# Optimization experiments

Hardware: AMD Instinct MI355X
Metric: run time of the kernel (lower is better)

Reference implementation:

```python
import jax, jax.numpy as jnp
import numpy as np

B, T, C, K = 16, 4096, 64, 1024  # K = codebook rows including pad row 0


def setup_inputs() -> dict:
    key = jax.random.key(0)
    k1, k2, k3 = jax.random.split(key, 3)
    z = jax.random.normal(k1, (B, T, C), dtype=jnp.float32)
    codebook_weight = jax.random.normal(k2, (K, C), dtype=jnp.float32)
    # contiguous valid prefixes of random length (torch loop breaks at first 0)
    lengths = jax.random.randint(k3, (B,), T // 2, T + 1)
    mask = (jnp.arange(T)[None, :] < lengths[:, None]).astype(jnp.float32)[:, :, None]
    return {"z": z, "codebook_weight": codebook_weight, "mask": mask}


def _forward(z, codebook_weight, mask):
    # F.normalize(z, p=2, dim=-1) with eps clamp
    z = z / jnp.clip(jnp.linalg.norm(z, axis=-1, keepdims=True), 1e-12)
    e = jax.lax.stop_gradient(codebook_weight)[1:]  # (K-1, C), detached like torch
    zf = z.reshape(-1, C)                            # (B*T, C)
    # squared euclidean distances: ||z||^2 + ||e||^2 - 2 z e^T
    d = (zf * zf).sum(1, keepdims=True) + (e * e).sum(1)[None, :] - 2.0 * (zf @ e.T)
    idx = jnp.argmin(d, axis=1).reshape(B, T)        # (B, T) codes in [0, K-2]
    # scatter(one-hot) @ e  ==  gather rows of e
    z_q = e[idx] * mask                              # (B, T, C)

    valid_count = mask.sum()
    commitment_loss = (jnp.square(z - jax.lax.stop_gradient(z_q)) * mask).sum() / valid_count

    # straight-through estimator
    z_q = z + z_q - jax.lax.stop_gradient(z)

    m1 = mask[:, 1:, :]
    smoothness_loss = (jnp.square(z_q[:, :-1, :] - z_q[:, 1:, :]) * m1).sum() / m1.sum()

    # --- parallel RLE (replaces the host-side python loop) ---
    # torch loop breaks at first mask==0 -> only contiguous valid prefix matters
    mvalid = jnp.cumprod(mask[..., 0], axis=1) > 0   # (B, T) bool
    change = idx[:, 1:] != idx[:, :-1]
    # position 0 always starts a segment; new segment where code changes inside valid prefix
    is_start = jnp.concatenate(
        [jnp.ones((B, 1), dtype=bool), change & mvalid[:, 1:]], axis=1)  # (B, T)
    # stable argsort puts start positions first, in increasing time order
    order = jnp.argsort(jnp.where(is_start, 0, 1), axis=1)               # (B, T)
    n = is_start.sum(axis=1)                                             # segments per batch
    sel_mask = jnp.arange(T)[None, :] < n[:, None]                        # (B, T)
    sel_pos = jnp.where(sel_mask, order, 0)                               # padded to T
    n_mask = sel_mask.astype(jnp.float32)[..., None]                      # (B, T, 1)
    n_z_q = jnp.take_along_axis(z_q, sel_pos[:, :, None], axis=1) * n_mask
    selected_encodings = jnp.where(
        sel_mask, jnp.take_along_axis(idx, sel_pos, axis=1) + 1, 0)       # (B, T) int
    return smoothness_loss, commitment_loss, z_q, n_z_q, n_mask, selected_encodings


def reference(z, codebook_weight, mask):
    return _forward(z, codebook_weight, mask)
```

## Files before the change

kernel.cpp:

```cpp
#include <hip/hip_runtime.h>
#include <math.h>

typedef __attribute__((ext_vector_type(8))) short short8;
typedef __attribute__((ext_vector_type(4))) float f32x4;

#define B_  16
#define T_  4096
#define C_  64
#define KE_ 1023
#define BT_ (B_ * T_)
#define WINHALF 5e-4f


__device__ __forceinline__ unsigned short f2bf(float x) {
    unsigned int u = __float_as_uint(x);
    unsigned int r = (u + 0x7FFFu + ((u >> 16) & 1u)) >> 16;
    return (unsigned short)r;
}
__device__ __forceinline__ float bf2f(unsigned short h) {
    return __uint_as_float(((unsigned int)h) << 16);
}

typedef __attribute__((address_space(1))) const unsigned int g_u32;
typedef __attribute__((address_space(3))) unsigned int l_u32;
__device__ __forceinline__ void gload16(const void* g, void* l) {
    __builtin_amdgcn_global_load_lds((g_u32*)g, (l_u32*)l, 16, 0, 0);
}

__global__ __launch_bounds__(256) void k_prep(const float* __restrict__ cb,
                                              float* __restrict__ ee,
                                              float* __restrict__ ee2,
                                              unsigned short* __restrict__ Eh,
                                              unsigned short* __restrict__ El,
                                              int* __restrict__ flagcnt) {
    const int gid = blockIdx.x * 256 + threadIdx.x;
    const int k = gid >> 5;
    const int c = gid & 31;
    if (gid == 0) *flagcnt = 0;
    unsigned int* EhU = (unsigned int*)Eh;
    unsigned int* ElU = (unsigned int*)El;
    if (k < KE_) {
        const float x0 = cb[(size_t)(k + 1) * C_ + 2 * c];
        const float x1 = cb[(size_t)(k + 1) * C_ + 2 * c + 1];
        const float n0 = -x0, n1 = -x1;
        const unsigned short h0 = f2bf(n0), h1 = f2bf(n1);
        const unsigned short l0 = f2bf(n0 - bf2f(h0));
        const unsigned short l1 = f2bf(n1 - bf2f(h1));
        EhU[k * 32 + c] = (unsigned int)h0 | ((unsigned int)h1 << 16);
        ElU[k * 32 + c] = (unsigned int)l0 | ((unsigned int)l1 << 16);
        if (c == 0) {
            const float* r = cb + (size_t)(k + 1) * C_;
            float s = 0.f;
            #pragma unroll
            for (int cc = 0; cc < C_; cc += 2) {
                const float y0 = r[cc], y1 = r[cc + 1];
                s = fmaf(y0, y0, s);
                s = fmaf(y1, y1, s);
            }
            ee[k]  = s;
            ee2[k] = 0.5f + 0.5f * s;
        }
    } else {
        EhU[k * 32 + c] = 0u;
        ElU[k * 32 + c] = 0u;
        if (c == 0) { ee[k] = INFINITY; ee2[k] = INFINITY; }
    }
}

__global__ __launch_bounds__(256, 2) void k_assign(
    const float* __restrict__ z, const unsigned short* __restrict__ Eh,
    const unsigned short* __restrict__ El, const float* __restrict__ ee2,
    int* __restrict__ kbest, int* __restrict__ flaglist,
    int* __restrict__ flagcnt) {

    __shared__ __align__(16) unsigned short s_eh[2][128 * 64];
    __shared__ __align__(16) unsigned short s_el[2][128 * 64];
    __shared__ float s_ee[2][128];

    const int tid  = threadIdx.x;
    const int wave = tid >> 6;
    const int lane = tid & 63;
    const int col  = lane & 15;
    const int quad = lane >> 4;
    const int Q0   = blockIdx.x * 128 + wave * 32;

    short8 ah[2][2], al[2][2];
    #pragma unroll
    for (int g = 0; g < 2; ++g) {
        const float4* zp = (const float4*)(z + (size_t)(Q0 + g * 16 + col) * C_);
        const float4 f0 = zp[quad * 2];
        const float4 f1 = zp[quad * 2 + 1];
        const float4 f2 = zp[8 + quad * 2];
        const float4 f3 = zp[8 + quad * 2 + 1];
        float xs[16] = {f0.x, f0.y, f0.z, f0.w, f1.x, f1.y, f1.z, f1.w,
                        f2.x, f2.y, f2.z, f2.w, f3.x, f3.y, f3.z, f3.w};
        float ss = 0.f;
        #pragma unroll
        for (int i = 0; i < 16; ++i) ss = fmaf(xs[i], xs[i], ss);
        ss += __shfl_xor(ss, 16);
        ss += __shfl_xor(ss, 32);
        const float inv = 1.f / fmaxf(sqrtf(ss), 1e-12f);
        short8 h0, h1, l0, l1;
        #pragma unroll
        for (int i = 0; i < 8; ++i) {
            const float x = xs[i] * inv;
            const unsigned short hx = f2bf(x);
            h0[i] = (short)hx;
            l0[i] = (short)f2bf(x - bf2f(hx));
            const float y = xs[8 + i] * inv;
            const unsigned short hy = f2bf(y);
            h1[i] = (short)hy;
            l1[i] = (short)f2bf(y - bf2f(hy));
        }
        ah[g][0] = h0; ah[g][1] = h1;
        al[g][0] = l0; al[g][1] = l1;
    }

    float bestv[2][4], secv[2][4];
    int   bkk[2][4];
    #pragma unroll
    for (int g = 0; g < 2; ++g)
        #pragma unroll
        for (int r = 0; r < 4; ++r) {
            bestv[g][r] = INFINITY; secv[g][r] = INFINITY; bkk[g][r] = 0;
        }

    const int srow = tid >> 3;
    const int schk = (tid & 7) ^ (srow & 7);
    const int ldsb = (wave * 8) * 64;

#define STAGE_J(tt, bb, j) do {                                                \
        const size_t go = (size_t)((tt) * 128 + (j) * 32 + srow) * 64          \
                          + (size_t)schk * 8;                                  \
        gload16(Eh + go, (void*)&s_eh[bb][ldsb + (j) * 2048]);                 \
        gload16(El + go, (void*)&s_el[bb][ldsb + (j) * 2048]);                 \
    } while (0)

    int cur = 0;
    #pragma unroll
    for (int j = 0; j < 4; ++j) STAGE_J(0, 0, j);
    if (tid < 128) s_ee[0][tid] = ee2[tid];
    __syncthreads();

    const int coff = (quad ^ (col & 7)) * 8;

    for (int t = 0; t < 8; ++t) {
        if (t < 7) { STAGE_J(t + 1, cur ^ 1, 0); STAGE_J(t + 1, cur ^ 1, 1); }

        float ev[8];
        #pragma unroll
        for (int s = 0; s < 8; ++s) ev[s] = s_ee[cur][s * 16 + col];

        short8 fh0 = *(const short8*)&s_eh[cur][col * 64 + coff];
        short8 fh1 = *(const short8*)&s_eh[cur][col * 64 + (coff ^ 32)];
        short8 fl0 = *(const short8*)&s_el[cur][col * 64 + coff];
        short8 fl1 = *(const short8*)&s_el[cur][col * 64 + (coff ^ 32)];

        if (t < 7) {
            STAGE_J(t + 1, cur ^ 1, 2); STAGE_J(t + 1, cur ^ 1, 3);
            if (tid < 128) s_ee[cur ^ 1][tid] = ee2[(t + 1) * 128 + tid];
        }

        const int kb = t * 128 + col;

        #pragma unroll
        for (int s = 0; s < 8; ++s) {
            const int sn = (s < 7) ? (s + 1) : 7;
            const int rb = (sn * 16 + col) * 64;
            short8 nh0 = *(const short8*)&s_eh[cur][rb + coff];
            short8 nh1 = *(const short8*)&s_eh[cur][rb + (coff ^ 32)];
            short8 nl0 = *(const short8*)&s_el[cur][rb + coff];
            short8 nl1 = *(const short8*)&s_el[cur][rb + (coff ^ 32)];

            const float e2 = ev[s];
            f32x4 p0a = {e2, e2, e2, e2}, p0b = {0.f, 0.f, 0.f, 0.f};
            f32x4 p1a = {e2, e2, e2, e2}, p1b = {0.f, 0.f, 0.f, 0.f};
            __builtin_amdgcn_s_setprio(1);
            p0a = __builtin_amdgcn_mfma_f32_16x16x32_bf16(ah[0][0], fh0, p0a, 0, 0, 0);
            p1a = __builtin_amdgcn_mfma_f32_16x16x32_bf16(ah[1][0], fh0, p1a, 0, 0, 0);
            p0b = __builtin_amdgcn_mfma_f32_16x16x32_bf16(ah[0][1], fl1, p0b, 0, 0, 0);
            p1b = __builtin_amdgcn_mfma_f32_16x16x32_bf16(ah[1][1], fl1, p1b, 0, 0, 0);
            p0a = __builtin_amdgcn_mfma_f32_16x16x32_bf16(ah[0][1], fh1, p0a, 0, 0, 0);
            p1a = __builtin_amdgcn_mfma_f32_16x16x32_bf16(ah[1][1], fh1, p1a, 0, 0, 0);
            p0b = __builtin_amdgcn_mfma_f32_16x16x32_bf16(al[0][0], fh0, p0b, 0, 0, 0);
            p1b = __builtin_amdgcn_mfma_f32_16x16x32_bf16(al[1][0], fh0, p1b, 0, 0, 0);
            p0a = __builtin_amdgcn_mfma_f32_16x16x32_bf16(ah[0][0], fl0, p0a, 0, 0, 0);
            p1a = __builtin_amdgcn_mfma_f32_16x16x32_bf16(ah[1][0], fl0, p1a, 0, 0, 0);
            p0b = __builtin_amdgcn_mfma_f32_16x16x32_bf16(al[0][1], fh1, p0b, 0, 0, 0);
            p1b = __builtin_amdgcn_mfma_f32_16x16x32_bf16(al[1][1], fh1, p1b, 0, 0, 0);
            __builtin_amdgcn_s_setprio(0);

            const int kc = kb + s * 16;
            #pragma unroll
            for (int r = 0; r < 4; ++r) {
                {
                    const float v  = p0a[r] + p0b[r];
                    const float bo = bestv[0][r];
                    bkk[0][r]   = (v < bo) ? kc : bkk[0][r];
                    secv[0][r]  = fminf(secv[0][r], fmaxf(bo, v));
                    bestv[0][r] = fminf(bo, v);
                }
                {
                    const float v  = p1a[r] + p1b[r];
                    const float bo = bestv[1][r];
                    bkk[1][r]   = (v < bo) ? kc : bkk[1][r];
                    secv[1][r]  = fminf(secv[1][r], fmaxf(bo, v));
                    bestv[1][r] = fminf(bo, v);
                }
            }
            fh0 = nh0; fh1 = nh1; fl0 = nl0; fl1 = nl1;
        }
        __syncthreads();
        cur ^= 1;
    }
#undef STAGE_J

    #pragma unroll
    for (int g = 0; g < 2; ++g) {
        #pragma unroll
        for (int r = 0; r < 4; ++r) {
            float b  = bestv[g][r], sc = secv[g][r];
            int   k  = bkk[g][r];
            #pragma unroll
            for (int off = 1; off < 16; off <<= 1) {
                const float ob = __shfl_xor(b, off);
                const int   ok = __shfl_xor(k, off);
                const float os = __shfl_xor(sc, off);
                const bool take = (ob < b) || (ob == b && ok < k);
                const float lose = take ? b : ob;
                sc = fminf(fminf(sc, os), lose);
                b  = take ? ob : b;
                k  = take ? ok : k;
            }
            if (col == 0) {
                const int q = Q0 + g * 16 + quad * 4 + r;
                kbest[q] = k;
                if (!(sc - b > WINHALF)) {
                    const int pos = atomicAdd(flagcnt, 1);
                    flaglist[pos] = q;
                }
            }
        }
    }
}

__global__ __launch_bounds__(256) void k_fix(const float* __restrict__ z,
                                             const float* __restrict__ cb,
                                             const float* __restrict__ ee,
                                             const int* __restrict__ flagcnt,
                                             const int* __restrict__ flaglist,
                                             int* __restrict__ kbest) {
    __shared__ float s_z[64];
    __shared__ float s_bv[4];
    __shared__ int   s_bk[4];
    const int tid  = threadIdx.x;
    const int lane = tid & 63;
    const int wave = tid >> 6;
    const int n = *flagcnt;

    for (int i = blockIdx.x; i < n; i += 1024) {
        const int q = flaglist[i];
        __syncthreads();
        if (tid < 16) ((float4*)s_z)[tid] = ((const float4*)(z + (size_t)q * C_))[tid];
        __syncthreads();

        float4 zn[16];
        float ss = 0.f;
        #pragma unroll
        for (int c4 = 0; c4 < 16; ++c4) {
            const float4 v = ((const float4*)s_z)[c4];
            zn[c4] = v;
            ss = fmaf(v.x, v.x, ss); ss = fmaf(v.y, v.y, ss);
            ss = fmaf(v.z, v.z, ss); ss = fmaf(v.w, v.w, ss);
        }
        const float nrm = fmaxf(sqrtf(ss), 1e-12f);
        #pragma unroll
        for (int c4 = 0; c4 < 16; ++c4) {
            zn[c4].x /= nrm; zn[c4].y /= nrm; zn[c4].z /= nrm; zn[c4].w /= nrm;
        }

        const int k0 = tid * 4;
        const float4* e0 = (const float4*)(cb + (size_t)(k0 + 1) * C_);
        const float4* e1 = (const float4*)(cb + (size_t)(k0 + 2) * C_);
        const float4* e2 = (const float4*)(cb + (size_t)(k0 + 3) * C_);
        const float4* e3 = (const float4*)(cb + (size_t)((k0 + 4 <= KE_) ? (k0 + 4) : KE_) * C_);
        float d0 = 0.f, d1 = 0.f, d2 = 0.f, d3 = 0.f;
        #pragma unroll
        for (int c4 = 0; c4 < 16; ++c4) {
            const float4 x = zn[c4];
            const float4 a = e0[c4], b = e1[c4], c = e2[c4], d = e3[c4];
            d0 = fmaf(x.x, a.x, d0); d0 = fmaf(x.y, a.y, d0);
            d0 = fmaf(x.z, a.z, d0); d0 = fmaf(x.w, a.w, d0);
            d1 = fmaf(x.x, b.x, d1); d1 = fmaf(x.y, b.y, d1);
            d1 = fmaf(x.z, b.z, d1); d1 = fmaf(x.w, b.w, d1);
            d2 = fmaf(x.x, c.x, d2); d2 = fmaf(x.y, c.y, d2);
            d2 = fmaf(x.z, c.z, d2); d2 = fmaf(x.w, c.w, d2);
            d3 = fmaf(x.x, d.x, d3); d3 = fmaf(x.y, d.y, d3);
            d3 = fmaf(x.z, d.z, d3); d3 = fmaf(x.w, d.w, d3);
        }
        float bv = INFINITY;
        int   bk = 0;
        float v;
        v = fmaf(-2.f, d0, ee[k0 + 0]); if (v < bv) { bv = v; bk = k0 + 0; }
        v = fmaf(-2.f, d1, ee[k0 + 1]); if (v < bv) { bv = v; bk = k0 + 1; }
        v = fmaf(-2.f, d2, ee[k0 + 2]); if (v < bv) { bv = v; bk = k0 + 2; }
        v = fmaf(-2.f, d3, ee[k0 + 3]); if (v < bv) { bv = v; bk = k0 + 3; }

        #pragma unroll
        for (int off = 32; off > 0; off >>= 1) {
            const float ov = __shfl_down(bv, off);
            const int   ok = __shfl_down(bk, off);
            if (ov < bv || (ov == bv && ok < bk)) { bv = ov; bk = ok; }
        }
        if (lane == 0) { s_bv[wave] = bv; s_bk[wave] = bk; }
        __syncthreads();
        if (tid == 0) {
            float fb = s_bv[0]; int fk = s_bk[0];
            #pragma unroll
            for (int w = 1; w < 4; ++w) {
                if (s_bv[w] < fb || (s_bv[w] == fb && s_bk[w] < fk)) {
                    fb = s_bv[w]; fk = s_bk[w];
                }
            }
            kbest[q] = fk;
        }
    }
}

__global__ __launch_bounds__(256) void k_episcan(
    const float* __restrict__ z, const float* __restrict__ cb,
    const float* __restrict__ mask, const int* __restrict__ kbest,
    float* __restrict__ zqo,
    float* __restrict__ commit_part, float* __restrict__ valid_part,
    float* __restrict__ smooth_part,
    int* __restrict__ selpos, int* __restrict__ nst) {

    const int tid = threadIdx.x;

    if (blockIdx.x < 16) {
        __shared__ int cnt[256];
        const int b = blockIdx.x;
        const int base = b * T_;
        const int t0 = tid * 16;

        int flags = 0, c = 0;
        int prev = (tid == 0) ? -1 : kbest[base + t0 - 1];
        #pragma unroll
        for (int i = 0; i < 16; ++i) {
            const int t = t0 + i;
            const int cur = kbest[base + t];
            const int is = (t == 0) ? 1
                         : ((cur != prev && mask[base + t] > 0.f) ? 1 : 0);
            flags |= is << i;
            c += is;
            prev = cur;
        }
        cnt[tid] = c;
        __syncthreads();
        for (int off = 1; off < 256; off <<= 1) {
            int add = (tid >= off) ? cnt[tid - off] : 0;
            __syncthreads();
            cnt[tid] += add;
            __syncthreads();
        }
        int pos = cnt[tid] - c;
        #pragma unroll
        for (int i = 0; i < 16; ++i) {
            if ((flags >> i) & 1) selpos[base + pos++] = t0 + i;
        }
        if (tid == 255) nst[b] = cnt[255];
        return;
    }

    __shared__ float s_red[12];
    const int bid  = blockIdx.x - 16;
    const int lane = tid & 63;
    const int wave = tid >> 6;
    const int gt   = bid * 256 + tid;
    const int q    = gt >> 2;
    const int p    = gt & 3;
    const int grp  = lane >> 2;

    const int bi = kbest[q];
    const float m = mask[q];

    const float4* zp = (const float4*)(z + (size_t)q * C_ + p * 16);
    const float4* er = (const float4*)(cb + (size_t)(bi + 1) * C_ + p * 16);
    float4* zo = (float4*)(zqo + (size_t)q * C_ + p * 16);

    float4 zr[4];
    float ss = 0.f;
    #pragma unroll
    for (int i = 0; i < 4; ++i) {
        float4 v = zp[i];
        zr[i] = v;
        ss = fmaf(v.x, v.x, ss); ss = fmaf(v.y, v.y, ss);
        ss = fmaf(v.z, v.z, ss); ss = fmaf(v.w, v.w, ss);
    }
    ss += __shfl_xor(ss, 1);
    ss += __shfl_xor(ss, 2);
    const float nrm = fmaxf(sqrtf(ss), 1e-12f);

    float commit = 0.f, sm = 0.f;
    float4 ov[4];
    #pragma unroll
    for (int c4 = 0; c4 < 4; ++c4) {
        const float z0 = zr[c4].x / nrm, z1 = zr[c4].y / nrm;
        const float z2 = zr[c4].z / nrm, z3 = zr[c4].w / nrm;
        const float4 e4 = er[c4];
        const float q0 = e4.x * m, q1 = e4.y * m, q2 = e4.z * m, q3 = e4.w * m;
        float4 o;
        o.x = (z0 + q0) - z0;
        o.y = (z1 + q1) - z1;
        o.z = (z2 + q2) - z2;
        o.w = (z3 + q3) - z3;
        zo[c4] = o;
        ov[c4] = o;
        const float d0 = z0 - q0, d1 = z1 - q1, d2 = z2 - q2, d3 = z3 - q3;
        commit = fmaf(d0, d0, commit); commit = fmaf(d1, d1, commit);
        commit = fmaf(d2, d2, commit); commit = fmaf(d3, d3, commit);
    }
    commit *= m;

    float mnext = 0.f;
    if (grp != 15) mnext = mask[q + 1];
    #pragma unroll
    for (int c4 = 0; c4 < 4; ++c4) {
        const float n0 = __shfl_down(ov[c4].x, 4);
        const float n1 = __shfl_down(ov[c4].y, 4);
        const float n2 = __shfl_down(ov[c4].z, 4);
        const float n3 = __shfl_down(ov[c4].w, 4);
        const float x0 = ov[c4].x - n0, x1 = ov[c4].y - n1;
        const float x2 = ov[c4].z - n2, x3 = ov[c4].w - n3;
        sm = fmaf(x0, x0, sm); sm = fmaf(x1, x1, sm);
        sm = fmaf(x2, x2, sm); sm = fmaf(x3, x3, sm);
    }
    sm *= mnext;

    if (grp == 15) {
        float mn = 0.f;
        if ((q & (T_ - 1)) != T_ - 1) mn = mask[q + 1];
        if (mn > 0.f) {
            const int bi2 = kbest[q + 1];
            const float4* zp2 = (const float4*)(z + (size_t)(q + 1) * C_ + p * 16);
            const float4* er2 = (const float4*)(cb + (size_t)(bi2 + 1) * C_ + p * 16);
            float4 zr2[4];
            float s2 = 0.f;
            #pragma unroll
            for (int i = 0; i < 4; ++i) {
                float4 v = zp2[i];
                zr2[i] = v;
                s2 = fmaf(v.x, v.x, s2); s2 = fmaf(v.y, v.y, s2);
                s2 = fmaf(v.z, v.z, s2); s2 = fmaf(v.w, v.w, s2);
            }
            s2 += __shfl_xor(s2, 1);
            s2 += __shfl_xor(s2, 2);
            const float nrm2 = fmaxf(sqrtf(s2), 1e-12f);
            float smb = 0.f;
            #pragma unroll
            for (int c4 = 0; c4 < 4; ++c4) {
                const float w0 = zr2[c4].x / nrm2, w1 = zr2[c4].y / nrm2;
                const float w2 = zr2[c4].z / nrm2, w3 = zr2[c4].w / nrm2;
                const float4 e4 = er2[c4];
                const float a0 = e4.x * mn, a1 = e4.y * mn;
                const float a2 = e4.z * mn, a3 = e4.w * mn;
                const float o0 = (w0 + a0) - w0;
                const float o1 = (w1 + a1) - w1;
                const float o2 = (w2 + a2) - w2;
                const float o3 = (w3 + a3) - w3;
                const float x0 = ov[c4].x - o0, x1 = ov[c4].y - o1;
                const float x2 = ov[c4].z - o2, x3 = ov[c4].w - o3;
                smb = fmaf(x0, x0, smb); smb = fmaf(x1, x1, smb);
                smb = fmaf(x2, x2, smb); smb = fmaf(x3, x3, smb);
            }
            sm = smb * mn;
        }
    }

    float vc = (p == 0) ? m : 0.f;
    #pragma unroll
    for (int off = 32; off > 0; off >>= 1) {
        commit += __shfl_down(commit, off);
        vc     += __shfl_down(vc, off);
        sm     += __shfl_down(sm, off);
    }
    if (lane == 0) { s_red[wave] = commit; s_red[4 + wave] = vc; s_red[8 + wave] = sm; }
    __syncthreads();
    if (tid == 0) {
        commit_part[bid] = s_red[0] + s_red[1] + s_red[2] + s_red[3];
        valid_part[bid]  = s_red[4] + s_red[5] + s_red[6] + s_red[7];
        smooth_part[bid] = s_red[8] + s_red[9] + s_red[10] + s_red[11];
    }
}

__global__ __launch_bounds__(256) void k_gsel(const float* __restrict__ zqo,
                                              const int* __restrict__ kbest,
                                              const int* __restrict__ selpos,
                                              const int* __restrict__ nst,
                                              const float* __restrict__ commit_part,
                                              const float* __restrict__ valid_part,
                                              const float* __restrict__ smooth_part,
                                              float* __restrict__ nzq,
                                              float* __restrict__ nmask,
                                              float* __restrict__ sel,
                                              float* __restrict__ out) {
    const int gid = blockIdx.x * 256 + threadIdx.x;
    const int b   = gid >> 16;
    const int rem = gid & 65535;
    const int j   = rem >> 4;
    const int c4  = rem & 15;
    const int n   = nst[b];
    float4 v = make_float4(0.f, 0.f, 0.f, 0.f);
    int p = 0;
    if (j < n) {
        p = selpos[b * T_ + j];
        v = ((const float4*)zqo)[((size_t)b * T_ + p) * 16 + c4];
    }
    ((float4*)nzq)[gid] = v;
    if (c4 == 0) {
        float nm = 0.f, s = 0.f;
        if (j < n) { nm = 1.f; s = (float)(kbest[b * T_ + p] + 1); }
        nmask[b * T_ + j] = nm;
        sel[b * T_ + j]   = s;
    }

    if (blockIdx.x == 0) {
        __shared__ double rc[256];
        __shared__ double rv[256];
        __shared__ double rs[256];
        const int tid = threadIdx.x;
        double sc = 0.0, sv = 0.0, ssm = 0.0;
        #pragma unroll
        for (int i = 0; i < 4; ++i) {
            sc  += (double)commit_part[tid + 256 * i];
            sv  += (double)valid_part[tid + 256 * i];
            ssm += (double)smooth_part[tid + 256 * i];
        }
        rc[tid] = sc; rv[tid] = sv; rs[tid] = ssm;
        __syncthreads();
        for (int off = 128; off > 0; off >>= 1) {
            if (tid < off) {
                rc[tid] += rc[tid + off];
                rv[tid] += rv[tid + off];
                rs[tid] += rs[tid + off];
            }
            __syncthreads();
        }
        if (tid == 0) {
            double valid = rv[0];
            out[0] = (float)(rs[0] / (valid - (double)B_));
            out[1] = (float)(rc[0] / valid);
        }
    }
}

extern "C" void kernel_launch(void* const* d_in, const int* in_sizes, int n_in,
                              void* d_out, int out_size, void* d_ws, size_t ws_size,
                              hipStream_t stream) {
    const float* z    = (const float*)d_in[0];
    const float* cb   = (const float*)d_in[1];
    const float* mask = (const float*)d_in[2];
    float* out = (float*)d_out;
    char* ws = (char*)d_ws;

    int*            flagcnt     = (int*)(ws + 0);
    float*          ee          = (float*)(ws + 64);
    unsigned short* Eh          = (unsigned short*)(ws + 4224);
    unsigned short* El          = (unsigned short*)(ws + 135296);
    int*            kbest       = (int*)(ws + 266368);
    int*            selpos      = (int*)(ws + 528512);
    int*            nst         = (int*)(ws + 790656);
    float*          commit_part = (float*)(ws + 791680);
    float*          valid_part  = (float*)(ws + 795776);
    float*          smooth_part = (float*)(ws + 799872);
    int*            flaglist    = (int*)(ws + 804032);
    float*          ee2         = (float*)(ws + 1066176);

    float* zqo   = out + 2;
    float* nzq   = zqo + (size_t)BT_ * C_;
    float* nmask = nzq + (size_t)BT_ * C_;
    float* sel   = nmask + BT_;

    k_prep   <<<128,  256, 0, stream>>>(cb, ee, ee2, Eh, El, flagcnt);
    k_assign <<<512,  256, 0, stream>>>(z, Eh, El, ee2, kbest, flaglist, flagcnt);
    k_fix    <<<1024, 256, 0, stream>>>(z, cb, ee, flagcnt, flaglist, kbest);
    k_episcan<<<1040, 256, 0, stream>>>(z, cb, mask, kbest, zqo,
                                        commit_part, valid_part, smooth_part,
                                        selpos, nst);
    k_gsel   <<<4096, 256, 0, stream>>>(zqo, kbest, selpos, nst,
                                        commit_part, valid_part, smooth_part,
                                        nzq, nmask, sel, out);
}
```

Baseline: 139.5 us.

## Triple-buffer codebook tiles with explicit vmcnt waits in assignment kernel

Reworks the codebook streaming in the nearest-code search from double-buffered 128-row tiles into triple-buffered 64-row tiles, prefetching two tiles ahead. Each iteration waits with a partial s_waitcnt vmcnt plus a raw s_barrier instead of a full __syncthreads. All codebook squared norms are preloaded into shared memory once. The aim is to hide global-to-LDS load latency behind the MFMA work and cut per-tile sync cost, at the price of twice as many barrier steps and fragile hand-counted waitcnt logic.

```diff
diff --git a/kernel.cpp b/kernel.cpp
--- a/kernel.cpp
+++ b/kernel.cpp
@@ -73,9 +73,9 @@
     int* __restrict__ kbest, int* __restrict__ flaglist,
     int* __restrict__ flagcnt) {
 
-    __shared__ __align__(16) unsigned short s_eh[2][128 * 64];
-    __shared__ __align__(16) unsigned short s_el[2][128 * 64];
-    __shared__ float s_ee[2][128];
+    __shared__ __align__(16) unsigned short s_eh[3][64 * 64];
+    __shared__ __align__(16) unsigned short s_el[3][64 * 64];
+    __shared__ float s_e2[1024];
 
     const int tid  = threadIdx.x;
     const int wave = tid >> 6;
@@ -127,45 +127,45 @@
 
     const int srow = tid >> 3;
     const int schk = (tid & 7) ^ (srow & 7);
-    const int ldsb = (wave * 8) * 64;
-
-#define STAGE_J(tt, bb, j) do {                                                \
-        const size_t go = (size_t)((tt) * 128 + (j) * 32 + srow) * 64          \
-                          + (size_t)schk * 8;                                  \
-        gload16(Eh + go, (void*)&s_eh[bb][ldsb + (j) * 2048]);                 \
-        gload16(El + go, (void*)&s_el[bb][ldsb + (j) * 2048]);                 \
+    const int ldsb = wave * 512;
+
+#define STAGE(tt, bb) do {                                                     \
+        _Pragma("unroll")                                                      \
+        for (int j = 0; j < 2; ++j) {                                          \
+            const size_t go = (size_t)((tt) * 64 + j * 32 + srow) * 64         \
+                              + (size_t)schk * 8;                              \
+            gload16(Eh + go, (void*)&s_eh[bb][ldsb + j * 2048]);               \
+            gload16(El + go, (void*)&s_el[bb][ldsb + j * 2048]);               \
+        }                                                                      \
     } while (0)
 
+    #pragma unroll
+    for (int i = 0; i < 4; ++i) s_e2[tid + 256 * i] = ee2[tid + 256 * i];
+    STAGE(0, 0);
+    STAGE(1, 1);
+    __syncthreads();
+
+    const int coff = (quad ^ (col & 7)) * 8;
+
     int cur = 0;
-    #pragma unroll
-    for (int j = 0; j < 4; ++j) STAGE_J(0, 0, j);
-    if (tid < 128) s_ee[0][tid] = ee2[tid];
-    __syncthreads();
-
-    const int coff = (quad ^ (col & 7)) * 8;
-
-    for (int t = 0; t < 8; ++t) {
-        if (t < 7) { STAGE_J(t + 1, cur ^ 1, 0); STAGE_J(t + 1, cur ^ 1, 1); }
-
-        float ev[8];
-        #pragma unroll
-        for (int s = 0; s < 8; ++s) ev[s] = s_ee[cur][s * 16 + col];
+    for (int t = 0; t < 16; ++t) {
+        const int nxt = (cur >= 1) ? cur - 1 : cur + 2;
+        if (t < 14) STAGE(t + 2, nxt);
+
+        float ev[4];
+        #pragma unroll
+        for (int s = 0; s < 4; ++s) ev[s] = s_e2[t * 64 + s * 16 + col];
 
         short8 fh0 = *(const short8*)&s_eh[cur][col * 64 + coff];
         short8 fh1 = *(const short8*)&s_eh[cur][col * 64 + (coff ^ 32)];
         short8 fl0 = *(const short8*)&s_el[cur][col * 64 + coff];
         short8 fl1 = *(const short8*)&s_el[cur][col * 64 + (coff ^ 32)];
 
-        if (t < 7) {
-            STAGE_J(t + 1, cur ^ 1, 2); STAGE_J(t + 1, cur ^ 1, 3);
-            if (tid < 128) s_ee[cur ^ 1][tid] = ee2[(t + 1) * 128 + tid];
-        }
-
-        const int kb = t * 128 + col;
-
-        #pragma unroll
-        for (int s = 0; s < 8; ++s) {
-            const int sn = (s < 7) ? (s + 1) : 7;
+        const int kb = t * 64 + col;
+
+        #pragma unroll
+        for (int s = 0; s < 4; ++s) {
+            const int sn = (s < 3) ? (s + 1) : 3;
             const int rb = (sn * 16 + col) * 64;
             short8 nh0 = *(const short8*)&s_eh[cur][rb + coff];
             short8 nh1 = *(const short8*)&s_eh[cur][rb + (coff ^ 32)];
@@ -210,10 +210,16 @@
             }
             fh0 = nh0; fh1 = nh1; fl0 = nl0; fl1 = nl1;
         }
-        __syncthreads();
-        cur ^= 1;
-    }
-#undef STAGE_J
+
+        if (t < 14) {
+            asm volatile("s_waitcnt vmcnt(4)");
+        } else if (t == 14) {
+            asm volatile("s_waitcnt vmcnt(0)");
+        }
+        if (t < 15) __builtin_amdgcn_s_barrier();
+        cur = (cur == 2) ? 0 : cur + 1;
+    }
+#undef STAGE
 
     #pragma unroll
     for (int g = 0; g < 2; ++g) {
```

Measured after the change: 140.2 us. No clear change (+0.5%).
